# Kernel optimization log

Hardware: AMD Instinct MI355X
Metric: run time of the kernel (lower is better)

The kernel has to match this reference:

```python
import math
import jax, jax.numpy as jnp
import numpy as np

# ---- module config (mirrors SE3PointTwoLayerKernel __init__) ----
RS_IN = [(4, 0), (4, 1), (4, 2)]
RS_OUT = [(4, 0), (4, 1), (4, 2)]
RADII = [0.5, 1.0, 1.5, 2.0]
HIDDEN = 10
J_MAX = 10
SIGMA = 0.6  # gaussian_radial_function default width
N_PTS = 256


def _cg(l1, m1, l2, m2, l3, m3):
    # Clebsch-Gordan <l3 m3 | l1 m1; l2 m2> (Condon-Shortley), Racah formula
    if m1 + m2 != m3:
        return 0.0
    f = math.factorial
    pre = math.sqrt((2 * l3 + 1) * f(l3 + l1 - l2) * f(l3 - l1 + l2) * f(l1 + l2 - l3) / f(l1 + l2 + l3 + 1))
    pre *= math.sqrt(f(l3 + m3) * f(l3 - m3) * f(l1 - m1) * f(l1 + m1) * f(l2 - m2) * f(l2 + m2))
    s = 0.0
    for k in range(l1 + l2 - l3 + 1):
        d = [k, l1 + l2 - l3 - k, l1 - m1 - k, l2 + m2 - k, l3 - l2 + m1 + k, l3 - l1 - m2 + k]
        if min(d) < 0:
            continue
        s += (-1) ** k / (f(d[0]) * f(d[1]) * f(d[2]) * f(d[3]) * f(d[4]) * f(d[5]))
    return pre * s


def _U_real(l):
    # unitary change of basis: Y_real = U @ Y_complex
    U = np.zeros((2 * l + 1, 2 * l + 1), dtype=np.complex128)
    U[l, l] = 1.0
    for m in range(1, l + 1):
        U[l + m, l + m] = (-1) ** m / math.sqrt(2)
        U[l + m, l - m] = 1 / math.sqrt(2)
        U[l - m, l + m] = -((-1) ** m) * 1j / math.sqrt(2)
        U[l - m, l - m] = 1j / math.sqrt(2)
    return U


def _Q_J(J, l_in, l_out):
    # basis_transformation_Q_J: real-basis equivariant coupling,
    # K[a, b] = sum_c Q[(a,b), c] * Yreal_J[c]
    CG = np.zeros((2 * l_out + 1, 2 * l_in + 1, 2 * J + 1))
    for mo in range(-l_out, l_out + 1):
        for mi in range(-l_in, l_in + 1):
            for mJ in range(-J, J + 1):
                CG[mo + l_out, mi + l_in, mJ + J] = _cg(l_in, mi, J, mJ, l_out, mo)
    T = np.einsum('ap,bq,cr,pqr->abc', _U_real(l_out), _U_real(l_in).conj(), _U_real(J).conj(), CG.astype(np.complex128))
    T = T.real if np.abs(T.real).sum() >= np.abs(T.imag).sum() else T.imag
    return np.ascontiguousarray(T.reshape((2 * l_out + 1) * (2 * l_in + 1), 2 * J + 1), dtype=np.float32)


def _build_paths():
    paths = []
    for (m_out, l_out) in RS_OUT:
        for (m_in, l_in) in RS_IN:
            Js = [J for J in range(abs(l_in - l_out), l_in + l_out + 1) if J <= J_MAX]
            paths.append((m_out, l_out, m_in, l_in, Js))
    return paths


PATHS = _build_paths()
NUM_PATHS = sum(1 for p in PATHS if len(p[4]) * len(RADII) > 0)
FILTER_IRREPS = sorted({J for p in PATHS for J in p[4]})
NW0 = sum(HIDDEN * len(RADII) * len(p[4]) for p in PATHS)
NB0 = HIDDEN * len(PATHS)
NW1 = sum(p[0] * p[2] * HIDDEN for p in PATHS)
NB1 = sum(p[0] * p[2] for p in PATHS)

Q_TABLES = {}
for (_mo, _lo, _mi, _li, _Js) in PATHS:
    for _J in _Js:
        if (_J, _li, _lo) not in Q_TABLES:
            Q_TABLES[(_J, _li, _lo)] = jnp.asarray(_Q_J(_J, _li, _lo))

Y_SLICES = {}
_off = 0
for _J in FILTER_IRREPS:
    Y_SLICES[_J] = slice(_off, _off + 2 * _J + 1)
    _off += 2 * _J + 1


def _real_sph_harm_xyz(ls, diff):
    # real spherical harmonics of unit directions, shape [sum(2l+1), N, M]
    eps = 1e-8
    r = jnp.sqrt(jnp.sum(diff * diff, axis=-1))
    rr = jnp.maximum(r, eps)
    x, y, z = diff[..., 0] / rr, diff[..., 1] / rr, diff[..., 2] / rr
    lmax = max(ls)
    A = [jnp.ones_like(z)]  # A_m = sin^m(theta) cos(m phi)
    B = [jnp.zeros_like(z)]  # B_m = sin^m(theta) sin(m phi)
    for m in range(1, lmax + 1):
        A.append(x * A[-1] - y * B[-1])
        B.append(x * B[-1] + y * A[-1])
    # P[l][m] = assoc. Legendre P_l^m(z) / sin^m(theta), CS-phase-free
    P = [[None] * (lmax + 1) for _ in range(lmax + 1)]
    P[0][0] = jnp.ones_like(z)
    for m in range(1, lmax + 1):
        P[m][m] = P[m - 1][m - 1] * (2 * m - 1)
    for m in range(lmax + 1):
        if m + 1 <= lmax:
            P[m + 1][m] = (2 * m + 1) * z * P[m][m]
        for l in range(m + 2, lmax + 1):
            P[l][m] = ((2 * l - 1) * z * P[l - 1][m] - (l - 1 + m) * P[l - 2][m]) / (l - m)
    rows = []
    for l in ls:
        for m in range(-l, l + 1):
            am = abs(m)
            Nc = math.sqrt((2 * l + 1) / (4 * math.pi) * math.factorial(l - am) / math.factorial(l + am))
            if m == 0:
                rows.append(Nc * P[l][0])
            elif m > 0:
                rows.append(math.sqrt(2) * Nc * P[l][m] * A[m])
            else:
                rows.append(math.sqrt(2) * Nc * P[l][am] * B[am])
    return jnp.stack(rows, axis=0)


def _forward(difference_mat, weight_0, biases_0, weight_1, biases_1):
    N, M, _ = difference_mat.shape
    Ys = jnp.asarray(_real_sph_harm_xyz(FILTER_IRREPS, difference_mat))  # [25, N, M]
    r_field = jnp.sqrt(jnp.sum(difference_mat * difference_mat, axis=-1))  # [N, M]
    norm = 1.0 / (SIGMA * math.sqrt(2 * math.pi))
    windows = [jnp.exp(-0.5 * ((r_field - r) / SIGMA) ** 2) * norm for r in RADII]
    w0i = b0i = w1i = b1i = 0
    pidx = 0
    row_blocks = []
    for (m_out, l_out) in RS_OUT:
        d_out = 2 * l_out + 1
        col_blocks = []
        for (m_in, l_in) in RS_IN:
            d_in = 2 * l_in + 1
            Js = PATHS[pidx][4]
            pidx += 1
            # angular basis K_J: [d_out, d_in, N, M]
            Ks = [jnp.einsum('mc,cnk->mnk', Q_TABLES[(J, l_in, l_out)], Ys[Y_SLICES[J]]).reshape(d_out, d_in, N, M) for J in Js]
            # radial x angular: [b_el, d_out, d_in, N, M], radii outer loop (matches torch)
            basis = jnp.stack([w[None, None] * K for w in windows for K in Ks], axis=0)
            b_el = basis.shape[0]
            fv0 = math.sqrt(d_out / (HIDDEN * b_el * NUM_PATHS))
            fv1 = math.sqrt(d_out / (m_in * HIDDEN * NUM_PATHS))
            w0 = (weight_0[w0i:w0i + HIDDEN * b_el] * fv0).reshape(HIDDEN, b_el)
            b0 = biases_0[b0i:b0i + HIDDEN]
            w1 = (weight_1[w1i:w1i + m_out * m_in * HIDDEN] * fv1).reshape(m_out * m_in, HIDDEN)
            b1 = biases_1[b1i:b1i + m_out * m_in]
            w0i += HIDDEN * b_el
        
            b0i += HIDDEN
            w1i += m_out * m_in * HIDDEN
            b1i += m_out * m_in
            h = jax.nn.relu(w0 @ basis.reshape(b_el, -1) + b0[:, None])
            ker = (w1 @ h + b1[:, None]).reshape(m_out, m_in, d_out, d_in, N, M)
            ker = ker.transpose(0, 2, 1, 3, 4, 5).reshape(m_out * d_out, m_in * d_in, N, M)
            col_blocks.append(ker)
        row_blocks.append(jnp.concatenate(col_blocks, axis=1))
    return jnp.concatenate(row_blocks, axis=0)


def setup_inputs():
    key = jax.random.key(0)
    k0, k1, k2, k3, k4 = jax.random.split(key, 5)
    return {
        'difference_mat': jax.random.normal(k0, (N_PTS, N_PTS, 3), dtype=jnp.float32),
        'weight_0': jax.random.normal(k1, (NW0,), dtype=jnp.float32),
        'biases_0': jax.random.normal(k2, (NB0,), dtype=jnp.float32) * 0.1,
        'weight_1': jax.random.normal(k3, (NW1,), dtype=jnp.float32),
        'biases_1': jax.random.normal(k4, (NB1,), dtype=jnp.float32) * 0.1,
    }


def reference(difference_mat, weight_0, biases_0, weight_1, biases_1):
    return _forward(difference_mat, weight_0, biases_0, weight_1, biases_1)
```

## Files before the change

kernel.cpp:

```cpp
#include <hip/hip_runtime.h>


#define DEV __device__ __forceinline__

constexpr int PW0[9]   = {0,40,80,120,160,280,400,440,560};
constexpr int PQOFF[9] = {0,1,10,35,44,125,350,375,600};
constexpr int YBASE[5] = {0,1,4,9,16};

__host__ __device__ constexpr int qlocal(int DO, int DI, int JS, int j) {
  int o = 0;
  for (int k = 0; k < j; ++k) o += DO * DI * (2 * (JS + k) + 1);
  return o;
}

__device__ double dfact(int n) { double f = 1.0; for (int i = 2; i <= n; ++i) f *= (double)i; return f; }

__device__ double cgc(int l1, int m1, int l2, int m2, int l3, int m3) {
  if (m1 + m2 != m3) return 0.0;
  double pre = sqrt((2.0 * l3 + 1.0) * dfact(l3 + l1 - l2) * dfact(l3 - l1 + l2) *
                    dfact(l1 + l2 - l3) / dfact(l1 + l2 + l3 + 1));
  pre *= sqrt(dfact(l3 + m3) * dfact(l3 - m3) * dfact(l1 - m1) * dfact(l1 + m1) *
              dfact(l2 - m2) * dfact(l2 + m2));
  double s = 0.0;
  for (int k = 0; k <= l1 + l2 - l3; ++k) {
    int d1 = l1 + l2 - l3 - k, d2 = l1 - m1 - k, d3 = l2 + m2 - k;
    int d4 = l3 - l2 + m1 + k, d5 = l3 - l1 - m2 + k;
    if (d1 < 0 || d2 < 0 || d3 < 0 || d4 < 0 || d5 < 0) continue;
    double term = 1.0 / (dfact(k) * dfact(d1) * dfact(d2) * dfact(d3) * dfact(d4) * dfact(d5));
    s += (k & 1) ? -term : term;
  }
  return pre * s;
}

__device__ int urow(int l, int a, int* col, double* re, double* im) {
  const double RS = 0.7071067811865476;
  int m = a - l;
  if (m == 0) { col[0] = l; re[0] = 1.0; im[0] = 0.0; return 1; }
  if (m > 0) {
    double s = (m & 1) ? -1.0 : 1.0;
    col[0] = l + m; re[0] = s * RS; im[0] = 0.0;
    col[1] = l - m; re[1] = RS;     im[1] = 0.0;
    return 2;
  }
  int mm = -m;
  double s = (mm & 1) ? -1.0 : 1.0;
  col[0] = l + mm; re[0] = 0.0; im[0] = -s * RS;
  col[1] = l - mm; re[1] = 0.0; im[1] = RS;
  return 2;
}

__global__ __launch_bounds__(256) void init_q_kernel(float* __restrict__ ws) {
  constexpr int T_LO[19]  = {0,0,0, 1, 1,1,1, 1,1,1, 2, 2,2,2, 2,2,2,2,2};
  constexpr int T_LI[19]  = {0,1,2, 0, 1,1,1, 2,2,2, 0, 1,1,1, 2,2,2,2,2};
  constexpr int T_J [19]  = {0,1,2, 1, 0,1,2, 1,2,3, 2, 1,2,3, 0,1,2,3,4};
  constexpr int T_OFF[19] = {0,1,10,35,44,53,80,125,170,245,350,375,420,495,600,625,700,825,1000};

  const int t  = blockIdx.x;
  const int lo = T_LO[t], li = T_LI[t], J = T_J[t];
  const int d_o = 2 * lo + 1, d_i = 2 * li + 1, w = 2 * J + 1;
  const int size = d_o * d_i * w;
  const int e = threadIdx.x;

  double tre = 0.0, tim = 0.0;
  if (e < size) {
    int row = e / w, cc = e % w;
    int a = row / d_i, b = row % d_i;
    int co[2], ci[2], cj[2];
    double ro[2], io[2], ri[2], ii[2], rj[2], ij[2];
    int no = urow(lo, a,  co, ro, io);
    int ni = urow(li, b,  ci, ri, ii);
    int nj = urow(J,  cc, cj, rj, ij);
    for (int i0 = 0; i0 < no; ++i0)
      for (int i1 = 0; i1 < ni; ++i1)
        for (int i2 = 0; i2 < nj; ++i2) {
          double cg = cgc(li, ci[i1] - li, J, cj[i2] - J, lo, co[i0] - lo);
          if (cg == 0.0) continue;
          double ar = ro[i0], ai = io[i0];
          double br = ri[i1], bi = -ii[i1];
          double cr = rj[i2], cii = -ij[i2];
          double abr = ar * br - ai * bi, abi = ar * bi + ai * br;
          double pr = abr * cr - abi * cii, pi = abr * cii + abi * cr;
          tre += pr * cg; tim += pi * cg;
        }
  }
  __shared__ double sre[256], sim[256];
  sre[threadIdx.x] = fabs(tre);
  sim[threadIdx.x] = fabs(tim);
  __syncthreads();
  for (int s = 128; s > 0; s >>= 1) {
    if (threadIdx.x < s) { sre[threadIdx.x] += sre[threadIdx.x + s]; sim[threadIdx.x] += sim[threadIdx.x + s]; }
    __syncthreads();
  }
  if (e < size) ws[T_OFF[t] + e] = (float)((sre[0] >= sim[0]) ? tre : tim);
}

template <int P>
DEV void do_path(const float* __restrict__ diff,
                 const float* __restrict__ w0g, const float* __restrict__ b0g,
                 const float* __restrict__ w1g, const float* __restrict__ b1g,
                 const float* __restrict__ Q, float* __restrict__ out,
                 int a0, int na, int n, int m) {
  constexpr int LO = P / 3, LI = P % 3;
  constexpr int DO = 2 * LO + 1, DI = 2 * LI + 1;
  constexpr int JS = (LO > LI) ? (LO - LI) : (LI - LO);
  constexpr int NJ = 2 * ((LO < LI) ? LO : LI) + 1;
  constexpr int BEL = 4 * NJ;
  constexpr int ROFF = (LO == 0) ? 0 : ((LO == 1) ? 4 : 16);
  constexpr int COFF = (LI == 0) ? 0 : ((LI == 1) ? 4 : 16);
  constexpr int W0OFF = PW0[P];
  constexpr int QOFF  = PQOFF[P];
  const float FV0 = sqrtf((float)DO / (10.0f * (float)BEL * 9.0f));
  const float FV1 = sqrtf((float)DO / 360.0f);

  const float* dp = diff + (((size_t)n << 8) + (size_t)m) * 3;
  const float dx = dp[0], dy = dp[1], dz = dp[2];
  const float r2 = dx * dx + dy * dy + dz * dz;
  const float r  = sqrtf(r2);
  const float rr = fmaxf(r, 1e-8f);
  const float inv = 1.0f / rr;
  const float x = dx * inv, y = dy * inv, z = dz * inv;

  float wv[4];
  {
    const float NORMC = 0.6649038006690546f;
    const float RAD[4] = {0.5f, 1.0f, 1.5f, 2.0f};
#pragma unroll
    for (int k = 0; k < 4; ++k) {
      float tq = (r - RAD[k]) * (1.0f / 0.6f);
      wv[k] = expf(-0.5f * tq * tq) * (NORMC * FV0);
    }
  }

  float Y[25];
  {
    const float A1 = x,                 B1 = y * A1;
    const float A2 = x * A1 - y * B1,   B2 = x * B1 + y * A2;
    const float A3 = x * A2 - y * B2,   B3 = x * B2 + y * A3;
    const float A4 = x * A3 - y * B3,   B4 = x * B3 + y * A4;
    const float z2 = z * z;
    Y[0]  = 0.28209479177387814f;
    Y[1]  = 0.4886025119029199f * B1;
    Y[2]  = 0.4886025119029199f * z;
    Y[3]  = 0.4886025119029199f * A1;
    Y[4]  = 0.5462742152960396f * B2;
    Y[5]  = 1.0925484305920792f * z * B1;
    Y[6]  = 0.31539156525252005f * (3.0f * z2 - 1.0f);
    Y[7]  = 1.0925484305920792f * z * A1;
    Y[8]  = 0.5462742152960396f * A2;
    Y[9]  = 0.5900435899266435f * B3;
    Y[10] = 1.445305721320277f * z * B2;
    Y[11] = 0.4570457994644658f * (5.0f * z2 - 1.0f) * B1;
    Y[12] = 0.3731763325901154f * z * (5.0f * z2 - 3.0f);
    Y[13] = 0.4570457994644658f * (5.0f * z2 - 1.0f) * A1;
    Y[14] = 1.445305721320277f * z * A2;
    Y[15] = 0.5900435899266435f * A3;
    Y[16] = 0.6258357354491761f * B4;
    Y[17] = 1.7701307697799304f * z * B3;
    Y[18] = 0.47308734787878004f * (7.0f * z2 - 1.0f) * B2;
    Y[19] = 0.6690465435572892f * z * (7.0f * z2 - 3.0f) * B1;
    Y[20] = 0.10578554691520431f * ((35.0f * z2 - 30.0f) * z2 + 3.0f);
    Y[21] = 0.6690465435572892f * z * (7.0f * z2 - 3.0f) * A1;
    Y[22] = 0.47308734787878004f * (7.0f * z2 - 1.0f) * A2;
    Y[23] = 1.7701307697799304f * z * A3;
    Y[24] = 0.6258357354491761f * A4;
  }

  float c[10][NJ];
#pragma unroll
  for (int t = 0; t < 10; ++t) {
#pragma unroll
    for (int j = 0; j < NJ; ++j) {
      float acc = 0.0f;
#pragma unroll
      for (int rx = 0; rx < 4; ++rx)
        acc = fmaf(w0g[W0OFF + t * BEL + rx * NJ + j], wv[rx], acc);
      c[t][j] = acc;
    }
  }
  float b0v[10];
#pragma unroll
  for (int t = 0; t < 10; ++t) b0v[t] = b0g[10 * P + t];

  float* __restrict__ outn = out + ((size_t)n << 8);
  const float* __restrict__ w1p = w1g + 160 * P;
  const float* __restrict__ b1p = b1g + 16 * P;

#pragma unroll 1
  for (int ai = 0; ai < na; ++ai) {
    const int a = a0 + ai;
#pragma unroll 1
    for (int b = 0; b < DI; ++b) {
      float K[NJ];
#pragma unroll
      for (int j = 0; j < NJ; ++j) {
        const int W = 2 * (JS + j) + 1;
        const int qbase = QOFF + qlocal(DO, DI, JS, j) + (a * DI + b) * W;
        float acc = 0.0f;
#pragma unroll
        for (int cc = 0; cc < 2 * (JS + j) + 1; ++cc)
          acc = fmaf(Q[qbase + cc], Y[YBASE[JS + j] + cc], acc);
        K[j] = acc;
      }
      float h[10];
#pragma unroll
      for (int t = 0; t < 10; ++t) {
        float acc = b0v[t];
#pragma unroll
        for (int j = 0; j < NJ; ++j) acc = fmaf(c[t][j], K[j], acc);
        h[t] = fmaxf(acc, 0.0f);
      }
#pragma unroll
      for (int u = 0; u < 4; ++u) {
        const int Rr = ROFF + u * DO + a;
#pragma unroll
        for (int v = 0; v < 4; ++v) {
          const int uv = u * 4 + v;
          float acc = 0.0f;
#pragma unroll
          for (int t = 0; t < 10; ++t)
            acc = fmaf(w1p[uv * 10 + t], h[t], acc);
          const float val = fmaf(acc, FV1, b1p[uv]);
          const int Cc = COFF + v * DI + b;
          float* __restrict__ op = outn + (((size_t)(Rr * 36 + Cc)) << 16);
          op[m] = val;
        }
      }
    }
  }
}

__global__ __launch_bounds__(256) void se3_all_kernel(
    const float* __restrict__ diff, const float* __restrict__ w0,
    const float* __restrict__ b0, const float* __restrict__ w1,
    const float* __restrict__ b1, const float* __restrict__ Q,
    float* __restrict__ out) {
  const int kind = blockIdx.x % 21;
  const int n    = blockIdx.x / 21;
  const int m    = threadIdx.x;
  switch (kind) {
    case 0: case 1: case 2: case 3: case 4:
      do_path<8>(diff, w0, b0, w1, b1, Q, out, kind, 1, n, m); break;
    case 5: case 6: case 7: case 8: case 9:
      do_path<7>(diff, w0, b0, w1, b1, Q, out, kind - 5, 1, n, m); break;
    case 10: case 11: case 12:
      do_path<5>(diff, w0, b0, w1, b1, Q, out, kind - 10, 1, n, m); break;
    case 13: case 14: case 15:
      do_path<4>(diff, w0, b0, w1, b1, Q, out, kind - 13, 1, n, m); break;
    case 16: do_path<0>(diff, w0, b0, w1, b1, Q, out, 0, 1, n, m); break;
    case 17: do_path<1>(diff, w0, b0, w1, b1, Q, out, 0, 1, n, m); break;
    case 18: do_path<2>(diff, w0, b0, w1, b1, Q, out, 0, 1, n, m); break;
    case 19: do_path<3>(diff, w0, b0, w1, b1, Q, out, 0, 3, n, m); break;
    case 20: do_path<6>(diff, w0, b0, w1, b1, Q, out, 0, 5, n, m); break;
  }
}

extern "C" void kernel_launch(void* const* d_in, const int* in_sizes, int n_in,
                              void* d_out, int out_size, void* d_ws, size_t ws_size,
                              hipStream_t stream) {
  const float* diff = (const float*)d_in[0];
  const float* w0   = (const float*)d_in[1];
  const float* b0   = (const float*)d_in[2];
  const float* w1   = (const float*)d_in[3];
  const float* b1   = (const float*)d_in[4];
  float* out = (float*)d_out;
  float* qws = (float*)d_ws;

  init_q_kernel<<<dim3(19), dim3(256), 0, stream>>>(qws);
  se3_all_kernel<<<dim3(21 * 256), dim3(256), 0, stream>>>(diff, w0, b0, w1, b1, qws, out);
}
```

Before: 448.1 us.

## Split into precompute stage for radial/Y features and per-(a,b) pair kernel

A first kernel computes the radial Gaussian weights and all 25 real spherical harmonics once per point pair and stores them in workspace planes. A second kernel launches one block per (n, output-element pair), 81 kinds, so each thread computes a single (a,b) entry with a smaller register footprint. The aim is to avoid recomputing geometry in every path block and to expose more parallelism with lower register pressure. In exchange it adds workspace traffic for 29 planes and repeats the hidden-layer MLP once per (a,b) pair instead of once per path. The old fused kernel remains as a fallback when the workspace is too small.

```diff
diff --git a/kernel.cpp b/kernel.cpp
--- a/kernel.cpp
+++ b/kernel.cpp
@@ -12,6 +12,9 @@
   for (int k = 0; k < j; ++k) o += DO * DI * (2 * (JS + k) + 1);
   return o;
 }
+
+constexpr int WSY = 2048;
+constexpr int PLANE = 65536;
 
 __device__ double dfact(int n) { double f = 1.0; for (int i = 2; i <= n; ++i) f *= (double)i; return f; }
 
@@ -94,6 +97,165 @@
   if (e < size) ws[T_OFF[t] + e] = (float)((sre[0] >= sim[0]) ? tre : tim);
 }
 
+__global__ __launch_bounds__(256) void se3_stage1(const float* __restrict__ diff,
+                                                  float* __restrict__ ws) {
+  const int n = blockIdx.x, m = threadIdx.x;
+  const int nm = (n << 8) | m;
+  const float* dp = diff + (size_t)nm * 3;
+  const float dx = dp[0], dy = dp[1], dz = dp[2];
+  const float r2 = dx * dx + dy * dy + dz * dz;
+  const float r  = sqrtf(r2);
+  const float rr = fmaxf(r, 1e-8f);
+  const float inv = 1.0f / rr;
+  const float x = dx * inv, y = dy * inv, z = dz * inv;
+
+  float* base = ws + WSY + nm;
+
+  {
+    const float NORMC = 0.6649038006690546f;
+    const float RAD[4] = {0.5f, 1.0f, 1.5f, 2.0f};
+#pragma unroll
+    for (int k = 0; k < 4; ++k) {
+      float tq = (r - RAD[k]) * (1.0f / 0.6f);
+      base[(size_t)k * PLANE] = expf(-0.5f * tq * tq) * NORMC;
+    }
+  }
+  {
+    const float A1 = x,                 B1 = y * A1;
+    const float A2 = x * A1 - y * B1,   B2 = x * B1 + y * A2;
+    const float A3 = x * A2 - y * B2,   B3 = x * B2 + y * A3;
+    const float A4 = x * A3 - y * B3,   B4 = x * B3 + y * A4;
+    const float z2 = z * z;
+    float Y[25];
+    Y[0]  = 0.28209479177387814f;
+    Y[1]  = 0.4886025119029199f * B1;
+    Y[2]  = 0.4886025119029199f * z;
+    Y[3]  = 0.4886025119029199f * A1;
+    Y[4]  = 0.5462742152960396f * B2;
+    Y[5]  = 1.0925484305920792f * z * B1;
+    Y[6]  = 0.31539156525252005f * (3.0f * z2 - 1.0f);
+    Y[7]  = 1.0925484305920792f * z * A1;
+    Y[8]  = 0.5462742152960396f * A2;
+    Y[9]  = 0.5900435899266435f * B3;
+    Y[10] = 1.445305721320277f * z * B2;
+    Y[11] = 0.4570457994644658f * (5.0f * z2 - 1.0f) * B1;
+    Y[12] = 0.3731763325901154f * z * (5.0f * z2 - 3.0f);
+    Y[13] = 0.4570457994644658f * (5.0f * z2 - 1.0f) * A1;
+    Y[14] = 1.445305721320277f * z * A2;
+    Y[15] = 0.5900435899266435f * A3;
+    Y[16] = 0.6258357354491761f * B4;
+    Y[17] = 1.7701307697799304f * z * B3;
+    Y[18] = 0.47308734787878004f * (7.0f * z2 - 1.0f) * B2;
+    Y[19] = 0.6690465435572892f * z * (7.0f * z2 - 3.0f) * B1;
+    Y[20] = 0.10578554691520431f * ((35.0f * z2 - 30.0f) * z2 + 3.0f);
+    Y[21] = 0.6690465435572892f * z * (7.0f * z2 - 3.0f) * A1;
+    Y[22] = 0.47308734787878004f * (7.0f * z2 - 1.0f) * A2;
+    Y[23] = 1.7701307697799304f * z * A3;
+    Y[24] = 0.6258357354491761f * A4;
+#pragma unroll
+    for (int i = 0; i < 25; ++i) base[(size_t)(4 + i) * PLANE] = Y[i];
+  }
+}
+
+template <int P>
+DEV void do_pair(const float* __restrict__ w0g, const float* __restrict__ b0g,
+                 const float* __restrict__ w1g, const float* __restrict__ b1g,
+                 const float* __restrict__ ws, float* __restrict__ out,
+                 int ab, int n, int m) {
+  constexpr int LO = P / 3, LI = P % 3;
+  constexpr int DO = 2 * LO + 1, DI = 2 * LI + 1;
+  constexpr int JS = (LO > LI) ? (LO - LI) : (LI - LO);
+  constexpr int NJ = 2 * ((LO < LI) ? LO : LI) + 1;
+  constexpr int BEL = 4 * NJ;
+  constexpr int ROFF = (LO == 0) ? 0 : ((LO == 1) ? 4 : 16);
+  constexpr int COFF = (LI == 0) ? 0 : ((LI == 1) ? 4 : 16);
+  constexpr int W0OFF = PW0[P];
+  constexpr int QOFF  = PQOFF[P];
+  constexpr int YLO = YBASE[JS];
+  constexpr int YHI = YBASE[JS + NJ - 1] + 2 * (JS + NJ - 1) + 1;
+  const float FV0 = sqrtf((float)DO / (10.0f * (float)BEL * 9.0f));
+  const float FV1 = sqrtf((float)DO / 360.0f);
+
+  const int nm = (n << 8) | m;
+  const float* __restrict__ sb = ws + WSY + nm;
+
+  float wvs[4];
+#pragma unroll
+  for (int k = 0; k < 4; ++k) wvs[k] = sb[(size_t)k * PLANE] * FV0;
+  float Yv[YHI - YLO];
+#pragma unroll
+  for (int i = 0; i < YHI - YLO; ++i) Yv[i] = sb[(size_t)(4 + YLO + i) * PLANE];
+
+  const int a = ab / DI, b = ab - a * DI;
+
+  const float* __restrict__ Q = ws;
+  float K[NJ];
+#pragma unroll
+  for (int j = 0; j < NJ; ++j) {
+    const int W = 2 * (JS + j) + 1;
+    const int qbase = QOFF + qlocal(DO, DI, JS, j) + ab * W;
+    float acc = 0.0f;
+#pragma unroll
+    for (int cc = 0; cc < 2 * (JS + j) + 1; ++cc)
+      acc = fmaf(Q[qbase + cc], Yv[YBASE[JS + j] - YLO + cc], acc);
+    K[j] = acc;
+  }
+
+  const float* __restrict__ b0p = b0g + 10 * P;
+  float h[10];
+#pragma unroll
+  for (int t = 0; t < 10; ++t) {
+    float acc = b0p[t];
+#pragma unroll
+    for (int j = 0; j < NJ; ++j) {
+      float cj = w0g[W0OFF + t * BEL + 0 * NJ + j] * wvs[0];
+#pragma unroll
+      for (int rx = 1; rx < 4; ++rx)
+        cj = fmaf(w0g[W0OFF + t * BEL + rx * NJ + j], wvs[rx], cj);
+      acc = fmaf(cj, K[j], acc);
+    }
+    h[t] = fmaxf(acc, 0.0f);
+  }
+
+  const float* __restrict__ w1p = w1g + 160 * P;
+  const float* __restrict__ b1p = b1g + 16 * P;
+  float* __restrict__ outn = out + ((size_t)n << 8);
+#pragma unroll
+  for (int u = 0; u < 4; ++u) {
+    const int Rr = ROFF + u * DO + a;
+#pragma unroll
+    for (int v = 0; v < 4; ++v) {
+      const int uv = u * 4 + v;
+      float acc = 0.0f;
+#pragma unroll
+      for (int t = 0; t < 10; ++t)
+        acc = fmaf(w1p[uv * 10 + t], h[t], acc);
+      const float val = fmaf(acc, FV1, b1p[uv]);
+      const int Cc = COFF + v * DI + b;
+      float* __restrict__ op = outn + (((size_t)(Rr * 36 + Cc)) << 16);
+      op[m] = val;
+    }
+  }
+}
+
+__global__ __launch_bounds__(256) void se3_stage2(
+    const float* __restrict__ w0, const float* __restrict__ b0,
+    const float* __restrict__ w1, const float* __restrict__ b1,
+    const float* __restrict__ ws, float* __restrict__ out) {
+  const int kind = blockIdx.x % 81;
+  const int n    = blockIdx.x / 81;
+  const int m    = threadIdx.x;
+  if      (kind < 1)  do_pair<0>(w0, b0, w1, b1, ws, out, kind,      n, m);
+  else if (kind < 4)  do_pair<1>(w0, b0, w1, b1, ws, out, kind - 1,  n, m);
+  else if (kind < 9)  do_pair<2>(w0, b0, w1, b1, ws, out, kind - 4,  n, m);
+  else if (kind < 12) do_pair<3>(w0, b0, w1, b1, ws, out, kind - 9,  n, m);
+  else if (kind < 21) do_pair<4>(w0, b0, w1, b1, ws, out, kind - 12, n, m);
+  else if (kind < 36) do_pair<5>(w0, b0, w1, b1, ws, out, kind - 21, n, m);
+  else if (kind < 41) do_pair<6>(w0, b0, w1, b1, ws, out, kind - 36, n, m);
+  else if (kind < 56) do_pair<7>(w0, b0, w1, b1, ws, out, kind - 41, n, m);
+  else                do_pair<8>(w0, b0, w1, b1, ws, out, kind - 56, n, m);
+}
+
 template <int P>
 DEV void do_path(const float* __restrict__ diff,
                  const float* __restrict__ w0g, const float* __restrict__ b0g,
@@ -130,7 +292,6 @@
       wv[k] = expf(-0.5f * tq * tq) * (NORMC * FV0);
     }
   }
-
   float Y[25];
   {
     const float A1 = x,                 B1 = y * A1;
@@ -266,5 +427,12 @@
   float* qws = (float*)d_ws;
 
   init_q_kernel<<<dim3(19), dim3(256), 0, stream>>>(qws);
-  se3_all_kernel<<<dim3(21 * 256), dim3(256), 0, stream>>>(diff, w0, b0, w1, b1, qws, out);
-}
+
+  const size_t NEED = (size_t)(WSY + 29 * PLANE) * sizeof(float);
+  if (ws_size >= NEED) {
+    se3_stage1<<<dim3(256), dim3(256), 0, stream>>>(diff, qws);
+    se3_stage2<<<dim3(81 * 256), dim3(256), 0, stream>>>(w0, b0, w1, b1, qws, out);
+  } else {
+    se3_all_kernel<<<dim3(21 * 256), dim3(256), 0, stream>>>(diff, w0, b0, w1, b1, qws, out);
+  }
+}
```

After: 387.6 us. 1.16x faster.
